# Kernel optimization log

Hardware: AMD Instinct MI355X
Metric: run time of the kernel (lower is better)

## Reference

```python
import jax, jax.numpy as jnp
import numpy as np

B, S, D = 2, 2048, 2048
H = 16
HD = D // H  # 128

def setup_inputs() -> dict:
    key = jax.random.key(0)
    k1, k2, k3 = jax.random.split(key, 3)
    x = jax.random.normal(k1, (B, S, D), dtype=jnp.float32)
    w_qkv = jax.random.normal(k2, (D, 3 * D), dtype=jnp.float32) * (1.0 / np.sqrt(D))
    b_qkv = jnp.zeros((3 * D,), dtype=jnp.float32)
    w_out = jax.random.normal(k3, (D, D), dtype=jnp.float32) * (1.0 / np.sqrt(D))
    b_out = jnp.zeros((D,), dtype=jnp.float32)
    return {"x": x, "w_qkv": w_qkv, "b_qkv": b_qkv, "w_out": w_out, "b_out": b_out}

def reference(x, w_qkv, b_qkv, w_out, b_out):
    batch, seq_len, channels = x.shape
    qkv = x @ w_qkv + b_qkv                      # [B,S,3D]
    q, k, v = jnp.split(qkv, 3, axis=-1)
    # [B,S,D] -> [B,H,S,HD]
    def heads(t):
        return t.reshape(batch, seq_len, H, HD).transpose(0, 2, 1, 3)
    q, k, v = heads(q), heads(k), heads(v)
    scale = 1.0 / np.sqrt(HD).astype(np.float32)
    attn = jnp.einsum('bhqd,bhkd->bhqk', q, k) * scale
    causal = jnp.tril(jnp.ones((seq_len, seq_len), dtype=bool))
    attn = jnp.where(causal, attn, -jnp.inf)
    attn = jax.nn.softmax(attn, axis=-1)
    y = jnp.einsum('bhqk,bhkd->bhqd', attn, v)   # [B,H,S,HD]
    y = y.transpose(0, 2, 1, 3).reshape(batch, seq_len, channels)
    return y @ w_out + b_out
```

## Files before the change

kernel.cpp:

```cpp
#include <hip/hip_runtime.h>
#include <hip/hip_bf16.h>
#include <cstdint>
#include <cstddef>

#define BB 2
#define SS 2048
#define DD 2048
#define HH 16
#define HDIM 128
#define QSCALE 0.12751743f

typedef short bf16x8 __attribute__((ext_vector_type(8)));
typedef float f32x4 __attribute__((ext_vector_type(4)));
typedef float f32x16 __attribute__((ext_vector_type(16)));

__device__ __forceinline__ ushort f2bf(float f) {
    union { float f; uint32_t u; } v; v.f = f;
    uint32_t u = v.u;
    u += 0x7fffu + ((u >> 16) & 1u);
    return (ushort)(u >> 16);
}

__device__ __forceinline__ ushort f2bf_fast(float f) {
    union { float f; uint32_t u; } v; v.f = f;
    return (ushort)((v.u + 0x8000u) >> 16);
}

__device__ __forceinline__ void gl16(const ushort* g, ushort* l) {
    __builtin_amdgcn_global_load_lds(
        (const __attribute__((address_space(1))) unsigned int*)g,
        (__attribute__((address_space(3))) unsigned int*)l,
        16, 0, 0);
}

__global__ __launch_bounds__(256) void cast_x_kernel(
    const float* __restrict__ X, ushort* __restrict__ Xb)
{
    size_t idx = ((size_t)blockIdx.x * 256 + threadIdx.x) * 8;
    float4 a = *(const float4*)(X + idx);
    float4 b = *(const float4*)(X + idx + 4);
    ushort4 o0, o1;
    o0.x = f2bf(a.x); o0.y = f2bf(a.y); o0.z = f2bf(a.z); o0.w = f2bf(a.w);
    o1.x = f2bf(b.x); o1.y = f2bf(b.y); o1.z = f2bf(b.z); o1.w = f2bf(b.w);
    *(ushort4*)(Xb + idx) = o0;
    *(ushort4*)(Xb + idx + 4) = o1;
}

__global__ __launch_bounds__(256) void transpose_cast_kernel(
    const float* __restrict__ W, ushort* __restrict__ Wt, int K, int N)
{
    __shared__ ushort tile[32][36];
    const int n0 = blockIdx.x * 32;
    const int k0 = blockIdx.y * 32;
    const int t = threadIdx.x;
    const int r = t >> 3;
    const int c = (t & 7) * 4;
    float4 a = *(const float4*)(W + (size_t)(k0 + r) * N + n0 + c);
    tile[r][c + 0] = f2bf(a.x); tile[r][c + 1] = f2bf(a.y);
    tile[r][c + 2] = f2bf(a.z); tile[r][c + 3] = f2bf(a.w);
    __syncthreads();
    ushort4 o;
    o.x = tile[c + 0][r]; o.y = tile[c + 1][r];
    o.z = tile[c + 2][r]; o.w = tile[c + 3][r];
    *(ushort4*)(Wt + (size_t)(n0 + r) * K + k0 + c) = o;
}

__global__ __launch_bounds__(256) void transpose_v_kernel(
    const ushort* __restrict__ V, ushort* __restrict__ Vt)
{
    __shared__ ushort tile[32][36];
    const int s0 = blockIdx.x * 32;
    const int h0 = blockIdx.y * 32;
    const int bh = blockIdx.z;
    const ushort* Vp = V + (size_t)bh * SS * HDIM;
    ushort* Vtp = Vt + (size_t)bh * HDIM * SS;
    const int t = threadIdx.x;
    const int r = t >> 3;
    const int c = (t & 7) * 4;
    *(ushort4*)&tile[r][c] = *(const ushort4*)(Vp + (size_t)(s0 + r) * HDIM + h0 + c);
    __syncthreads();
    ushort4 o;
    o.x = tile[c + 0][r]; o.y = tile[c + 1][r];
    o.z = tile[c + 2][r]; o.w = tile[c + 3][r];
    *(ushort4*)(Vtp + (size_t)(h0 + r) * SS + s0 + c) = o;
}

__global__ __launch_bounds__(256) void gemm_qkv_kernel(
    const ushort* __restrict__ A, const ushort* __restrict__ Bt,
    const float* __restrict__ bias,
    ushort* __restrict__ Qo, ushort* __restrict__ Ko, ushort* __restrict__ Vo)
{
    const int n0 = blockIdx.x * 128;
    const int m0 = blockIdx.y * 128;
    __shared__ ushort As[128 * 32];
    __shared__ ushort Bs[128 * 32];
    const int t = threadIdx.x, w = t >> 6, lane = t & 63;
    const int l31 = lane & 31, hh = lane >> 5;
    const int lrow = lane >> 2, lks = lane & 3;
    const int wr = w >> 1, wc = w & 1;
    const int swst = (lrow >> 1) & 3;
    const int swr  = (l31 >> 1) & 3;

    f32x16 acc[2][2];
#pragma unroll
    for (int i = 0; i < 2; ++i)
#pragma unroll
        for (int j = 0; j < 2; ++j) acc[i][j] = (f32x16)0.f;

    for (int k0 = 0; k0 < DD; k0 += 32) {
        __syncthreads();
#pragma unroll
        for (int q = 0; q < 2; ++q) {
            int e = w * 2 + q;
            int row = e * 16 + lrow;
            gl16(A  + (size_t)(m0 + row) * DD + k0 + (lks ^ swst) * 8, &As[e * 512]);
            gl16(Bt + (size_t)(n0 + row) * DD + k0 + (lks ^ swst) * 8, &Bs[e * 512]);
        }
        __syncthreads();
#pragma unroll
        for (int k16 = 0; k16 < 2; ++k16) {
            int co = ((k16 * 2 + hh) ^ swr) * 8;
            bf16x8 ar0 = *(const bf16x8*)&As[(wr * 64 + l31) * 32 + co];
            bf16x8 ar1 = *(const bf16x8*)&As[(wr * 64 + 32 + l31) * 32 + co];
            bf16x8 br0 = *(const bf16x8*)&Bs[(wc * 64 + l31) * 32 + co];
            bf16x8 br1 = *(const bf16x8*)&Bs[(wc * 64 + 32 + l31) * 32 + co];
            acc[0][0] = __builtin_amdgcn_mfma_f32_32x32x16_bf16(ar0, br0, acc[0][0], 0, 0, 0);
            acc[0][1] = __builtin_amdgcn_mfma_f32_32x32x16_bf16(ar0, br1, acc[0][1], 0, 0, 0);
            acc[1][0] = __builtin_amdgcn_mfma_f32_32x32x16_bf16(ar1, br0, acc[1][0], 0, 0, 0);
            acc[1][1] = __builtin_amdgcn_mfma_f32_32x32x16_bf16(ar1, br1, acc[1][1], 0, 0, 0);
        }
    }

    const int bidx = m0 >> 11;
    const int which = n0 >> 11;
    ushort* dst = (which == 0) ? Qo : ((which == 1) ? Ko : Vo);
    const float sc = (which == 0) ? QSCALE : 1.0f;
#pragma unroll
    for (int j = 0; j < 2; ++j) {
        int n = n0 + wc * 64 + j * 32 + l31;
        int c = n & 2047, h = c >> 7, hd = c & 127;
        float bv = bias[n];
        size_t base = ((size_t)(bidx * HH + h) * SS) * HDIM + hd;
#pragma unroll
        for (int i = 0; i < 2; ++i) {
#pragma unroll
            for (int r = 0; r < 16; ++r) {
                int s = (m0 & 2047) + wr * 64 + i * 32 + (r & 3) + 8 * (r >> 2) + 4 * hh;
                dst[base + (size_t)s * HDIM] = f2bf((acc[i][j][r] + bv) * sc);
            }
        }
    }
}

__global__ __launch_bounds__(256) void gemm_out_kernel(
    const ushort* __restrict__ A, const ushort* __restrict__ Bt,
    const float* __restrict__ bias, float* __restrict__ Out)
{
    const int n0 = blockIdx.x * 128;
    const int m0 = blockIdx.y * 128;
    __shared__ ushort As[128 * 32];
    __shared__ ushort Bs[128 * 32];
    const int t = threadIdx.x, w = t >> 6, lane = t & 63;
    const int l31 = lane & 31, hh = lane >> 5;
    const int lrow = lane >> 2, lks = lane & 3;
    const int wr = w >> 1, wc = w & 1;
    const int swst = (lrow >> 1) & 3;
    const int swr  = (l31 >> 1) & 3;

    f32x16 acc[2][2];
#pragma unroll
    for (int i = 0; i < 2; ++i)
#pragma unroll
        for (int j = 0; j < 2; ++j) acc[i][j] = (f32x16)0.f;

    for (int k0 = 0; k0 < DD; k0 += 32) {
        __syncthreads();
#pragma unroll
        for (int q = 0; q < 2; ++q) {
            int e = w * 2 + q;
            int row = e * 16 + lrow;
            gl16(A  + (size_t)(m0 + row) * DD + k0 + (lks ^ swst) * 8, &As[e * 512]);
            gl16(Bt + (size_t)(n0 + row) * DD + k0 + (lks ^ swst) * 8, &Bs[e * 512]);
        }
        __syncthreads();
#pragma unroll
        for (int k16 = 0; k16 < 2; ++k16) {
            int co = ((k16 * 2 + hh) ^ swr) * 8;
            bf16x8 ar0 = *(const bf16x8*)&As[(wr * 64 + l31) * 32 + co];
            bf16x8 ar1 = *(const bf16x8*)&As[(wr * 64 + 32 + l31) * 32 + co];
            bf16x8 br0 = *(const bf16x8*)&Bs[(wc * 64 + l31) * 32 + co];
            bf16x8 br1 = *(const bf16x8*)&Bs[(wc * 64 + 32 + l31) * 32 + co];
            acc[0][0] = __builtin_amdgcn_mfma_f32_32x32x16_bf16(ar0, br0, acc[0][0], 0, 0, 0);
            acc[0][1] = __builtin_amdgcn_mfma_f32_32x32x16_bf16(ar0, br1, acc[0][1], 0, 0, 0);
            acc[1][0] = __builtin_amdgcn_mfma_f32_32x32x16_bf16(ar1, br0, acc[1][0], 0, 0, 0);
            acc[1][1] = __builtin_amdgcn_mfma_f32_32x32x16_bf16(ar1, br1, acc[1][1], 0, 0, 0);
        }
    }

#pragma unroll
    for (int j = 0; j < 2; ++j) {
        int n = n0 + wc * 64 + j * 32 + l31;
        float bv = bias[n];
#pragma unroll
        for (int i = 0; i < 2; ++i) {
#pragma unroll
            for (int r = 0; r < 16; ++r) {
                int m = m0 + wr * 64 + i * 32 + (r & 3) + 8 * (r >> 2) + 4 * hh;
                Out[(size_t)m * DD + n] = acc[i][j][r] + bv;
            }
        }
    }
}

__global__ __launch_bounds__(256, 2) void attn_mfma_kernel(
    const ushort* __restrict__ Q, const ushort* __restrict__ K,
    const ushort* __restrict__ Vt, ushort* __restrict__ Y)
{
    const int bh = blockIdx.y;
    const int qt = gridDim.x - 1 - blockIdx.x;
    const int q0 = qt * 128;
    const int b = bh >> 4, h = bh & 15;

    __shared__ ushort Ks[2][4 * 64 * 32];
    __shared__ ushort Vs[2][2 * 128 * 32];

    const int t = threadIdx.x, w = t >> 6, lane = t & 63;
    const int l31 = lane & 31, hh = lane >> 5;
    const int lrow = lane >> 2, lks = lane & 3;
    const int swst = (lrow >> 1) & 3;
    const int swr  = (l31 >> 1) & 3;

    const ushort* Qp = Q  + (size_t)bh * SS * HDIM;
    const ushort* Kp = K  + (size_t)bh * SS * HDIM;
    const ushort* Vp = Vt + (size_t)bh * HDIM * SS;

    bf16x8 aq[8];
#pragma unroll
    for (int kb2 = 0; kb2 < 8; ++kb2)
        aq[kb2] = *(const bf16x8*)(Qp + (size_t)(q0 + w * 32 + l31) * HDIM + kb2 * 16 + hh * 8);

    bf16x8 ones;
#pragma unroll
    for (int j = 0; j < 8; ++j) ones[j] = (short)0x3F80;

    f32x16 O[4];
#pragma unroll
    for (int nt = 0; nt < 4; ++nt) O[nt] = (f32x16)0.f;
    f32x16 Ol = (f32x16)0.f;

    const int kbdiag = 2 * qt + (w >> 1);
    const int nkb = 2 * qt + 2;
    const bool hi = (hh == 1);
    const int qg = q0 + w * 32 + l31;

#define STAGE_KV(kb_, s_) do {                                                  \
    const int kbase_ = (kb_) * 64;                                              \
    _Pragma("unroll")                                                           \
    for (int g = 0; g < 4; ++g) {                                               \
        int key = g * 16 + lrow;                                                \
        gl16(Kp + (size_t)(kbase_ + key) * HDIM + w * 32 + (lks ^ swst) * 8,    \
             &Ks[s_][w * 2048 + g * 512]);                                      \
    }                                                                           \
    _Pragma("unroll")                                                           \
    for (int g = 0; g < 4; ++g) {                                               \
        int pan = g >> 1, sub = g & 1;                                          \
        int dim = w * 32 + sub * 16 + lrow;                                     \
        gl16(Vp + (size_t)dim * SS + kbase_ + pan * 32 + (lks ^ swst) * 8,      \
             &Vs[s_][pan * 4096 + (w * 32 + sub * 16) * 32]);                   \
    }                                                                           \
} while (0)

    STAGE_KV(0, 0);

    for (int kb = 0; kb < nkb; ++kb) {
        const int kbase = kb * 64;
        const int slot = kb & 1;

        if (kb + 1 < nkb) {
            STAGE_KV(kb + 1, slot ^ 1);
            asm volatile("s_waitcnt vmcnt(8)" ::: "memory");
        } else {
            asm volatile("s_waitcnt vmcnt(0)" ::: "memory");
        }
        __builtin_amdgcn_s_barrier();

        const ushort* KsS = Ks[slot];
        const ushort* VsS = Vs[slot];

        if (kb <= kbdiag) {
            f32x16 st0 = (f32x16)0.f, st1 = (f32x16)0.f;
            __builtin_amdgcn_s_setprio(1);
#pragma unroll
            for (int kb2 = 0; kb2 < 8; ++kb2) {
                int co = (((kb2 & 1) * 2 + hh) ^ swr) * 8;
                bf16x8 bk0 = *(const bf16x8*)&KsS[(kb2 >> 1) * 2048 + l31 * 32 + co];
                bf16x8 bk1 = *(const bf16x8*)&KsS[(kb2 >> 1) * 2048 + (32 + l31) * 32 + co];
                st0 = __builtin_amdgcn_mfma_f32_32x32x16_bf16(bk0, aq[kb2], st0, 0, 0, 0);
                st1 = __builtin_amdgcn_mfma_f32_32x32x16_bf16(bk1, aq[kb2], st1, 0, 0, 0);
            }
            __builtin_amdgcn_s_setprio(0);

            if (kb == kbdiag) {
#pragma unroll
                for (int r = 0; r < 16; ++r) {
                    int keyr = kbase + (r & 3) + 8 * (r >> 2) + 4 * hh;
                    if (keyr > qg)      st0[r] = -1e30f;
                    if (keyr + 32 > qg) st1[r] = -1e30f;
                }
            }

#pragma unroll
            for (int half = 0; half < 2; ++half) {
                float p[16];
#pragma unroll
                for (int r = 0; r < 16; ++r)
                    p[r] = __builtin_amdgcn_exp2f((half == 0) ? st0[r] : st1[r]);
                uint w0[4], w1[4];
#pragma unroll
                for (int g = 0; g < 4; ++g) {
                    w0[g] = (uint)f2bf_fast(p[4 * g])
                          | ((uint)f2bf_fast(p[4 * g + 1]) << 16);
                    w1[g] = (uint)f2bf_fast(p[4 * g + 2])
                          | ((uint)f2bf_fast(p[4 * g + 3]) << 16);
                }
#pragma unroll
                for (int kblk2 = 0; kblk2 < 2; ++kblk2) {
                    uint own0 = hi ? w0[2 * kblk2 + 1] : w0[2 * kblk2];
                    uint own1 = hi ? w1[2 * kblk2 + 1] : w1[2 * kblk2];
                    uint snd0 = hi ? w0[2 * kblk2]     : w0[2 * kblk2 + 1];
                    uint snd1 = hi ? w1[2 * kblk2]     : w1[2 * kblk2 + 1];
                    uint ps0 = (uint)__shfl_xor((int)snd0, 32, 64);
                    uint ps1 = (uint)__shfl_xor((int)snd1, 32, 64);
                    union { uint u[4]; bf16x8 v; } fr;
                    fr.u[0] = hi ? ps0 : own0;
                    fr.u[1] = hi ? ps1 : own1;
                    fr.u[2] = hi ? own0 : ps0;
                    fr.u[3] = hi ? own1 : ps1;
                    int co = ((kblk2 * 2 + hh) ^ swr) * 8;
                    __builtin_amdgcn_s_setprio(1);
#pragma unroll
                    for (int nt = 0; nt < 4; ++nt) {
                        bf16x8 bv = *(const bf16x8*)&VsS[half * 4096 + (nt * 32 + l31) * 32 + co];
                        O[nt] = __builtin_amdgcn_mfma_f32_32x32x16_bf16(fr.v, bv, O[nt], 0, 0, 0);
                    }
                    Ol = __builtin_amdgcn_mfma_f32_32x32x16_bf16(fr.v, ones, Ol, 0, 0, 0);
                    __builtin_amdgcn_s_setprio(0);
                }
            }
        }
        __builtin_amdgcn_s_barrier();
    }
#undef STAGE_KV

#pragma unroll
    for (int r = 0; r < 16; ++r) {
        int s = q0 + w * 32 + (r & 3) + 8 * (r >> 2) + 4 * hh;
        float inv = 1.0f / Ol[r];
        size_t base = ((size_t)(b * SS + s)) * DD + h * HDIM;
#pragma unroll
        for (int nt = 0; nt < 4; ++nt)
            Y[base + nt * 32 + l31] = f2bf(O[nt][r] * inv);
    }
}

extern "C" void kernel_launch(void* const* d_in, const int* in_sizes, int n_in,
                              void* d_out, int out_size, void* d_ws, size_t ws_size,
                              hipStream_t stream) {
    const float* x     = (const float*)d_in[0];
    const float* w_qkv = (const float*)d_in[1];
    const float* b_qkv = (const float*)d_in[2];
    const float* w_out = (const float*)d_in[3];
    const float* b_out = (const float*)d_in[4];
    float* out = (float*)d_out;

    ushort* ws  = (ushort*)d_ws;
    ushort* xb  = ws;
    ushort* wtq = xb + 8388608;
    ushort* wto = wtq + 12582912;
    ushort* q   = wto + 4194304;
    ushort* k   = q + 8388608;
    ushort* v   = k + 8388608;
    ushort* vt  = v + 8388608;
    ushort* y   = vt + 8388608;

    cast_x_kernel<<<4096, 256, 0, stream>>>(x, xb);
    transpose_cast_kernel<<<dim3(192, 64), 256, 0, stream>>>(w_qkv, wtq, DD, 3 * DD);
    transpose_cast_kernel<<<dim3(64, 64), 256, 0, stream>>>(w_out, wto, DD, DD);
    gemm_qkv_kernel<<<dim3(48, 32), 256, 0, stream>>>(xb, wtq, b_qkv, q, k, v);
    transpose_v_kernel<<<dim3(64, 4, 32), 256, 0, stream>>>(v, vt);
    attn_mfma_kernel<<<dim3(16, 32), 256, 0, stream>>>(q, k, vt, y);
    gemm_out_kernel<<<dim3(16, 32), 256, 0, stream>>>(y, wto, b_out, out);
}
```

Measured before the change: 406.4 us.

## Double GEMM K-tile to 64 and reorder attention block scheduling

```diff
diff --git a/kernel.cpp b/kernel.cpp
--- a/kernel.cpp
+++ b/kernel.cpp
@@ -92,14 +92,18 @@
 {
     const int n0 = blockIdx.x * 128;
     const int m0 = blockIdx.y * 128;
-    __shared__ ushort As[128 * 32];
-    __shared__ ushort Bs[128 * 32];
+    __shared__ ushort As[128 * 64];
+    __shared__ ushort Bs[128 * 64];
     const int t = threadIdx.x, w = t >> 6, lane = t & 63;
     const int l31 = lane & 31, hh = lane >> 5;
-    const int lrow = lane >> 2, lks = lane & 3;
     const int wr = w >> 1, wc = w & 1;
-    const int swst = (lrow >> 1) & 3;
-    const int swr  = (l31 >> 1) & 3;
+    const int swr = (l31 >> 1) & 3;
+
+    const int rt   = lane >> 3;
+    const int kh   = (lane >> 2) & 1;
+    const int ch   = lane & 3;
+    const int skey = (lane >> 4) & 3;
+    const int koff = kh * 32 + ((ch ^ skey) * 8);
 
     f32x16 acc[2][2];
 #pragma unroll
@@ -107,23 +111,22 @@
 #pragma unroll
         for (int j = 0; j < 2; ++j) acc[i][j] = (f32x16)0.f;
 
-    for (int k0 = 0; k0 < DD; k0 += 32) {
+    for (int k0 = 0; k0 < DD; k0 += 64) {
         __syncthreads();
 #pragma unroll
-        for (int q = 0; q < 2; ++q) {
-            int e = w * 2 + q;
-            int row = e * 16 + lrow;
-            gl16(A  + (size_t)(m0 + row) * DD + k0 + (lks ^ swst) * 8, &As[e * 512]);
-            gl16(Bt + (size_t)(n0 + row) * DD + k0 + (lks ^ swst) * 8, &Bs[e * 512]);
+        for (int q = 0; q < 4; ++q) {
+            int R = (w * 4 + q) * 8 + rt;
+            gl16(A  + (size_t)(m0 + R) * DD + k0 + koff, &As[(w * 4 + q) * 512]);
+            gl16(Bt + (size_t)(n0 + R) * DD + k0 + koff, &Bs[(w * 4 + q) * 512]);
         }
         __syncthreads();
 #pragma unroll
-        for (int k16 = 0; k16 < 2; ++k16) {
-            int co = ((k16 * 2 + hh) ^ swr) * 8;
-            bf16x8 ar0 = *(const bf16x8*)&As[(wr * 64 + l31) * 32 + co];
-            bf16x8 ar1 = *(const bf16x8*)&As[(wr * 64 + 32 + l31) * 32 + co];
-            bf16x8 br0 = *(const bf16x8*)&Bs[(wc * 64 + l31) * 32 + co];
-            bf16x8 br1 = *(const bf16x8*)&Bs[(wc * 64 + 32 + l31) * 32 + co];
+        for (int k16 = 0; k16 < 4; ++k16) {
+            int co = (k16 >> 1) * 32 + ((((k16 & 1) * 2 + hh) ^ swr) * 8);
+            bf16x8 ar0 = *(const bf16x8*)&As[(wr * 64 + l31) * 64 + co];
+            bf16x8 ar1 = *(const bf16x8*)&As[(wr * 64 + 32 + l31) * 64 + co];
+            bf16x8 br0 = *(const bf16x8*)&Bs[(wc * 64 + l31) * 64 + co];
+            bf16x8 br1 = *(const bf16x8*)&Bs[(wc * 64 + 32 + l31) * 64 + co];
             acc[0][0] = __builtin_amdgcn_mfma_f32_32x32x16_bf16(ar0, br0, acc[0][0], 0, 0, 0);
             acc[0][1] = __builtin_amdgcn_mfma_f32_32x32x16_bf16(ar0, br1, acc[0][1], 0, 0, 0);
             acc[1][0] = __builtin_amdgcn_mfma_f32_32x32x16_bf16(ar1, br0, acc[1][0], 0, 0, 0);
@@ -158,14 +161,18 @@
 {
     const int n0 = blockIdx.x * 128;
     const int m0 = blockIdx.y * 128;
-    __shared__ ushort As[128 * 32];
-    __shared__ ushort Bs[128 * 32];
+    __shared__ ushort As[128 * 64];
+    __shared__ ushort Bs[128 * 64];
     const int t = threadIdx.x, w = t >> 6, lane = t & 63;
     const int l31 = lane & 31, hh = lane >> 5;
-    const int lrow = lane >> 2, lks = lane & 3;
     const int wr = w >> 1, wc = w & 1;
-    const int swst = (lrow >> 1) & 3;
-    const int swr  = (l31 >> 1) & 3;
+    const int swr = (l31 >> 1) & 3;
+
+    const int rt   = lane >> 3;
+    const int kh   = (lane >> 2) & 1;
+    const int ch   = lane & 3;
+    const int skey = (lane >> 4) & 3;
+    const int koff = kh * 32 + ((ch ^ skey) * 8);
 
     f32x16 acc[2][2];
 #pragma unroll
@@ -173,23 +180,22 @@
 #pragma unroll
         for (int j = 0; j < 2; ++j) acc[i][j] = (f32x16)0.f;
 
-    for (int k0 = 0; k0 < DD; k0 += 32) {
+    for (int k0 = 0; k0 < DD; k0 += 64) {
         __syncthreads();
 #pragma unroll
-        for (int q = 0; q < 2; ++q) {
-            int e = w * 2 + q;
-            int row = e * 16 + lrow;
-            gl16(A  + (size_t)(m0 + row) * DD + k0 + (lks ^ swst) * 8, &As[e * 512]);
-            gl16(Bt + (size_t)(n0 + row) * DD + k0 + (lks ^ swst) * 8, &Bs[e * 512]);
+        for (int q = 0; q < 4; ++q) {
+            int R = (w * 4 + q) * 8 + rt;
+            gl16(A  + (size_t)(m0 + R) * DD + k0 + koff, &As[(w * 4 + q) * 512]);
+            gl16(Bt + (size_t)(n0 + R) * DD + k0 + koff, &Bs[(w * 4 + q) * 512]);
         }
         __syncthreads();
 #pragma unroll
-        for (int k16 = 0; k16 < 2; ++k16) {
-            int co = ((k16 * 2 + hh) ^ swr) * 8;
-            bf16x8 ar0 = *(const bf16x8*)&As[(wr * 64 + l31) * 32 + co];
-            bf16x8 ar1 = *(const bf16x8*)&As[(wr * 64 + 32 + l31) * 32 + co];
-            bf16x8 br0 = *(const bf16x8*)&Bs[(wc * 64 + l31) * 32 + co];
-            bf16x8 br1 = *(const bf16x8*)&Bs[(wc * 64 + 32 + l31) * 32 + co];
+        for (int k16 = 0; k16 < 4; ++k16) {
+            int co = (k16 >> 1) * 32 + ((((k16 & 1) * 2 + hh) ^ swr) * 8);
+            bf16x8 ar0 = *(const bf16x8*)&As[(wr * 64 + l31) * 64 + co];
+            bf16x8 ar1 = *(const bf16x8*)&As[(wr * 64 + 32 + l31) * 64 + co];
+            bf16x8 br0 = *(const bf16x8*)&Bs[(wc * 64 + l31) * 64 + co];
+            bf16x8 br1 = *(const bf16x8*)&Bs[(wc * 64 + 32 + l31) * 64 + co];
             acc[0][0] = __builtin_amdgcn_mfma_f32_32x32x16_bf16(ar0, br0, acc[0][0], 0, 0, 0);
             acc[0][1] = __builtin_amdgcn_mfma_f32_32x32x16_bf16(ar0, br1, acc[0][1], 0, 0, 0);
             acc[1][0] = __builtin_amdgcn_mfma_f32_32x32x16_bf16(ar1, br0, acc[1][0], 0, 0, 0);
@@ -216,8 +222,10 @@
     const ushort* __restrict__ Q, const ushort* __restrict__ K,
     const ushort* __restrict__ Vt, ushort* __restrict__ Y)
 {
-    const int bh = blockIdx.y;
-    const int qt = gridDim.x - 1 - blockIdx.x;
+    const int fid = blockIdx.x;
+    const int halfg = fid >> 8, rg = fid & 255;
+    const int qt = halfg ? (rg & 15) : (15 - (rg & 15));
+    const int bh = (halfg << 4) | (rg >> 4);
     const int q0 = qt * 128;
     const int b = bh >> 4, h = bh & 15;
 
@@ -388,6 +396,6 @@
     transpose_cast_kernel<<<dim3(64, 64), 256, 0, stream>>>(w_out, wto, DD, DD);
     gemm_qkv_kernel<<<dim3(48, 32), 256, 0, stream>>>(xb, wtq, b_qkv, q, k, v);
     transpose_v_kernel<<<dim3(64, 4, 32), 256, 0, stream>>>(v, vt);
-    attn_mfma_kernel<<<dim3(16, 32), 256, 0, stream>>>(q, k, vt, y);
+    attn_mfma_kernel<<<dim3(512), 256, 0, stream>>>(q, k, vt, y);
     gemm_out_kernel<<<dim3(16, 32), 256, 0, stream>>>(y, wto, b_out, out);
 }
```

After: 374.5 us. 7.9% less time.
